# Performance work log

Measured on AMD Instinct MI355X. Metric: run time of the kernel, lower is better.

Reference implementation:

```python
import jax, jax.numpy as jnp
import numpy as np

KS = 3   # kernel_size = sqrt(window_size=9)
PAD = 1  # KS // 2


def _unfold(t):
    # F.unfold(t, kernel_size=3, padding=1) then view(B,C,K,HW).permute(0,3,2,1)
    # -> (B, HW, K, C), K enumerated row-major over the 3x3 window.
    B, C, H, W = t.shape
    tp = jnp.pad(t, ((0, 0), (0, 0), (PAD, PAD), (PAD, PAD)))
    patches = jnp.stack(
        [tp[:, :, i:i + H, j:j + W] for i in range(KS) for j in range(KS)],
        axis=2,
    )  # (B, C, K, H, W)
    return patches.reshape(B, C, KS * KS, H * W).transpose(0, 3, 2, 1)


def setup_inputs() -> dict:
    key = jax.random.key(0)
    ks = jax.random.split(key, 8)
    B, C, H, W = 8, 256, 64, 64
    Cr = C // 8  # reduction=8
    return {
        "x": jax.random.normal(ks[0], (B, C, H, W), dtype=jnp.float32),
        "Wq": jax.random.normal(ks[1], (Cr, C), dtype=jnp.float32) * 0.02,
        "bq": jax.random.normal(ks[2], (Cr,), dtype=jnp.float32) * 0.02,
        "Wk": jax.random.normal(ks[3], (Cr, C), dtype=jnp.float32) * 0.02,
        "bk": jax.random.normal(ks[4], (Cr,), dtype=jnp.float32) * 0.02,
        "Wv": jax.random.normal(ks[5], (C, C), dtype=jnp.float32) * 0.02,
        "bv": jax.random.normal(ks[6], (C,), dtype=jnp.float32) * 0.02,
        "gamma": jax.random.normal(ks[7], (1,), dtype=jnp.float32) * 0.1,
    }


def reference(x, Wq, bq, Wk, bk, Wv, bv, gamma):
    B, C, H, W = x.shape
    # 1x1 convs == per-pixel linear projections
    q = jnp.einsum('bchw,oc->bohw', x, Wq) + bq[None, :, None, None]
    k = jnp.einsum('bchw,oc->bohw', x, Wk) + bk[None, :, None, None]
    v = jnp.einsum('bchw,oc->bohw', x, Wv) + bv[None, :, None, None]
    ku = _unfold(k)  # (B, HW, K, Cr)
    vu = _unfold(v)  # (B, HW, K, C)
    qf = q.reshape(B, -1, H * W).transpose(0, 2, 1)  # (B, HW, Cr)
    energy = jnp.einsum('bqc,bqkc->bqk', qf, ku)     # (B, HW, K)
    attn = jax.nn.softmax(energy, axis=-1)
    out = jnp.einsum('bqk,bqkc->bqc', attn, vu)      # (B, HW, C)
    out = out.transpose(0, 2, 1).reshape(B, C, H, W)
    return gamma * out + x
```

## Files before the change

### kernel.cpp

```cpp
#include <hip/hip_runtime.h>

#define HW   4096
#define HIMG 64
#define WIMG 64
#define CC   256
#define CR   32
#define B_   8

typedef __attribute__((ext_vector_type(8))) short bf16x8;
typedef __attribute__((ext_vector_type(4))) float f32x4;

__device__ inline unsigned short f2bf(float f) {
    union { float f; unsigned u; } v; v.f = f;
    return (unsigned short)((v.u + 0x8000u) >> 16);
}
__device__ inline float bf2f(unsigned short h) {
    union { unsigned u; float f; } v; v.u = ((unsigned)h) << 16; return v.f;
}
__device__ inline unsigned pack2(float a, float b) {
    return (unsigned)f2bf(a) | ((unsigned)f2bf(b) << 16);
}

__global__ __launch_bounds__(256) void wconv(
    const float* __restrict__ Wq, const float* __restrict__ bq,
    const float* __restrict__ Wk, const float* __restrict__ bk,
    const float* __restrict__ Wv, const float* __restrict__ bv,
    unsigned short* __restrict__ Wb, float* __restrict__ bb)
{
    const int o = blockIdx.x;
    const float* src; const float* bsrc; int orel;
    if (o < 32)      { src = Wq; bsrc = bq; orel = o;      }
    else if (o < 64) { src = Wk; bsrc = bk; orel = o - 32; }
    else             { src = Wv; bsrc = bv; orel = o - 64; }
    Wb[o * CC + threadIdx.x] = f2bf(src[orel * CC + threadIdx.x]);
    if (threadIdx.x == 0) bb[o] = bsrc[orel];
}

__global__ __launch_bounds__(256) void proj_gemm(
    const unsigned short* __restrict__ Wb, const float* __restrict__ bb,
    const float* __restrict__ x,
    float* __restrict__ q, float* __restrict__ k,
    unsigned short* __restrict__ vv)
{
    __shared__ unsigned short As[320 * 72];
    __shared__ float          xt32[64 * 65];
    __shared__ unsigned short Bs[64 * 64];

    const int b   = blockIdx.y;
    const int hw0 = blockIdx.x * 64;
    const int t    = threadIdx.x;
    const int lane = t & 63, wv = t >> 6;
    const int m16  = lane & 15, quad = lane >> 4;

    f32x4 acc[5][4];
    #pragma unroll
    for (int i = 0; i < 5; ++i)
        #pragma unroll
        for (int n = 0; n < 4; ++n)
            acc[i][n] = (f32x4){0.f, 0.f, 0.f, 0.f};

    for (int kc = 0; kc < 4; ++kc) {
        const int k0 = kc * 64;
        if (kc) __syncthreads();

        #pragma unroll
        for (int i = 0; i < 10; ++i) {
            int idx = t + 256 * i;
            int row = idx >> 3, s8 = idx & 7;
            *(uint4*)&As[row * 72 + s8 * 8] =
                *(const uint4*)&Wb[row * CC + k0 + s8 * 8];
        }
        #pragma unroll
        for (int i = 0; i < 4; ++i) {
            int idx = t + 256 * i;
            int c = idx >> 4, p4 = (idx & 15) * 4;
            float4 vx = *(const float4*)&x[((size_t)b * CC + k0 + c) * HW + hw0 + p4];
            *(float4*)&xt32[c * 65 + p4] = vx;
        }
        __syncthreads();

        {
            const int px = lane;
            const int c0 = wv * 16;
            float f[16];
            #pragma unroll
            for (int j = 0; j < 16; ++j)
                f[j] = xt32[(c0 + j) * 65 + px];
            uint4 w0, w1;
            w0.x = pack2(f[0],  f[1]);  w0.y = pack2(f[2],  f[3]);
            w0.z = pack2(f[4],  f[5]);  w0.w = pack2(f[6],  f[7]);
            w1.x = pack2(f[8],  f[9]);  w1.y = pack2(f[10], f[11]);
            w1.z = pack2(f[12], f[13]); w1.w = pack2(f[14], f[15]);
            const int lg0 = c0 >> 3, sw = px & 7;
            *(uint4*)&Bs[px * 64 + ((lg0     ^ sw) * 8)] = w0;
            *(uint4*)&Bs[px * 64 + (((lg0+1) ^ sw) * 8)] = w1;
        }
        __syncthreads();

        #pragma unroll
        for (int ks = 0; ks < 2; ++ks) {
            bf16x8 af[5], bf[4];
            #pragma unroll
            for (int i = 0; i < 5; ++i)
                af[i] = *(const bf16x8*)&As[((wv * 5 + i) * 16 + m16) * 72
                                            + ks * 32 + quad * 8];
            #pragma unroll
            for (int n = 0; n < 4; ++n) {
                int px = n * 16 + m16;
                int lg = ks * 4 + quad;
                bf[n] = *(const bf16x8*)&Bs[px * 64 + ((lg ^ (px & 7)) * 8)];
            }
            #pragma unroll
            for (int i = 0; i < 5; ++i)
                #pragma unroll
                for (int n = 0; n < 4; ++n)
                    acc[i][n] = __builtin_amdgcn_mfma_f32_16x16x32_bf16(
                        af[i], bf[n], acc[i][n], 0, 0, 0);
        }
    }

    #pragma unroll
    for (int i = 0; i < 5; ++i) {
        const int ob = (wv * 5 + i) * 16;
        #pragma unroll
        for (int r = 0; r < 4; ++r) {
            const int orow = quad * 4 + r;
            const float bias = bb[ob + orow];
            if (ob < 64) {
                float* dst = (ob < 32) ? q : k;
                int orel = (ob < 32) ? ob : ob - 32;
                size_t rowbase = ((size_t)b * CR + orel + orow) * HW;
                #pragma unroll
                for (int n = 0; n < 4; ++n)
                    dst[rowbase + hw0 + n * 16 + m16] = acc[i][n][r] + bias;
            } else {
                size_t rowbase = ((size_t)b * CC + (ob - 64) + orow) * HW;
                #pragma unroll
                for (int n = 0; n < 4; ++n)
                    vv[rowbase + hw0 + n * 16 + m16] = f2bf(acc[i][n][r] + bias);
            }
        }
    }
}

__global__ __launch_bounds__(256) void attn_w(
    const float* __restrict__ q_, const float* __restrict__ k_,
    float* __restrict__ aw)
{
    __shared__ float qs[64][33];
    __shared__ float ks[3][64][33];
    __shared__ float es[64][9];
    const int h = blockIdx.x, b = blockIdx.y, t = threadIdx.x;

    #pragma unroll
    for (int i = 0; i < 2; ++i) {
        int idx = t + 256 * i, cr = idx >> 4, p4 = (idx & 15) * 4;
        float4 vq = *(const float4*)&q_[((size_t)b * CR + cr) * HW + h * WIMG + p4];
        qs[p4 + 0][cr] = vq.x; qs[p4 + 1][cr] = vq.y;
        qs[p4 + 2][cr] = vq.z; qs[p4 + 3][cr] = vq.w;
    }
    #pragma unroll
    for (int r = 0; r < 3; ++r) {
        int hh = h + r - 1;
        bool ok = (hh >= 0) && (hh < HIMG);
        #pragma unroll
        for (int i = 0; i < 2; ++i) {
            int idx = t + 256 * i, cr = idx >> 4, p4 = (idx & 15) * 4;
            float4 vk = make_float4(0.f, 0.f, 0.f, 0.f);
            if (ok)
                vk = *(const float4*)&k_[((size_t)b * CR + cr) * HW + hh * WIMG + p4];
            ks[r][p4 + 0][cr] = vk.x; ks[r][p4 + 1][cr] = vk.y;
            ks[r][p4 + 2][cr] = vk.z; ks[r][p4 + 3][cr] = vk.w;
        }
    }
    __syncthreads();

    for (int id = t; id < 576; id += 256) {
        int px = id / 9, kk = id - px * 9;
        int di = kk / 3, dj = kk - di * 3;
        int hh = h + di - 1, ww = px + dj - 1;
        float e = 0.f;
        if (hh >= 0 && hh < HIMG && ww >= 0 && ww < WIMG) {
            float s = 0.f;
            #pragma unroll
            for (int c = 0; c < CR; ++c) s = fmaf(qs[px][c], ks[di][ww][c], s);
            e = s;
        }
        es[px][kk] = e;
    }
    __syncthreads();

    if (t < 64) {
        float m = es[t][0];
        #pragma unroll
        for (int kk = 1; kk < 9; ++kk) m = fmaxf(m, es[t][kk]);
        float ex[9]; float ssum = 0.f;
        #pragma unroll
        for (int kk = 0; kk < 9; ++kk) { ex[kk] = __expf(es[t][kk] - m); ssum += ex[kk]; }
        float inv = 1.f / ssum;
        float* dst = &aw[((size_t)b * HW + h * WIMG + t) * 12];
        #pragma unroll
        for (int kk = 0; kk < 9; ++kk) dst[kk] = ex[kk] * inv;
    }
}

__global__ __launch_bounds__(256) void apply(
    const float* __restrict__ x, const unsigned short* __restrict__ vv,
    const float* __restrict__ aw, const float* __restrict__ gamma,
    float* __restrict__ out)
{
    __shared__ float vs[3][32][73];
    __shared__ float aws[64][13];
    const int h = blockIdx.x, cb = blockIdx.y, b = blockIdx.z, t = threadIdx.x;

    for (int p = t; p < 768; p += 256) {
        int px = p / 12, kk = p - px * 12;
        aws[px][kk] = aw[((size_t)b * HW + h * WIMG) * 12 + p];
    }
    #pragma unroll
    for (int i = 0; i < 6; ++i) {
        int idx = t + 256 * i;
        int p4 = (idx & 15) * 4, c = (idx >> 4) & 31, r = idx >> 9;
        int hh = h + r - 1;
        float4 val = make_float4(0.f, 0.f, 0.f, 0.f);
        if (hh >= 0 && hh < HIMG) {
            ushort4 u = *(const ushort4*)&vv[((size_t)b * CC + cb * 32 + c) * HW
                                             + hh * WIMG + p4];
            val = make_float4(bf2f(u.x), bf2f(u.y), bf2f(u.z), bf2f(u.w));
        }
        float* dstp = &vs[r][c][4 + p4];
        dstp[0] = val.x; dstp[1] = val.y; dstp[2] = val.z; dstp[3] = val.w;
    }
    if (t < 96) {
        int r = t >> 5, c = t & 31;
        float* row = &vs[r][c][0];
        row[0] = 0.f; row[1] = 0.f; row[2] = 0.f; row[3] = 0.f;
        row[68] = 0.f; row[69] = 0.f; row[70] = 0.f; row[71] = 0.f;
    }
    __syncthreads();

    const int px0 = (t & 15) * 4;
    const int cl  = t >> 4;
    float w[4][9];
    #pragma unroll
    for (int i = 0; i < 4; ++i)
        #pragma unroll
        for (int kk = 0; kk < 9; ++kk) w[i][kk] = aws[px0 + i][kk];
    const float g = gamma[0];

    #pragma unroll
    for (int ci = 0; ci < 2; ++ci) {
        int c = cl + 16 * ci;
        float a0 = 0.f, a1 = 0.f, a2 = 0.f, a3 = 0.f;
        #pragma unroll
        for (int r = 0; r < 3; ++r) {
            const float* row = &vs[r][c][0];
            float lft = row[3 + px0];
            float c0  = row[4 + px0];
            float c1  = row[5 + px0];
            float c2  = row[6 + px0];
            float c3  = row[7 + px0];
            float rgt = row[8 + px0];
            int r3 = r * 3;
            a0 = fmaf(w[0][r3], lft, fmaf(w[0][r3+1], c0, fmaf(w[0][r3+2], c1, a0)));
            a1 = fmaf(w[1][r3], c0,  fmaf(w[1][r3+1], c1, fmaf(w[1][r3+2], c2, a1)));
            a2 = fmaf(w[2][r3], c1,  fmaf(w[2][r3+1], c2, fmaf(w[2][r3+2], c3, a2)));
            a3 = fmaf(w[3][r3], c2,  fmaf(w[3][r3+1], c3, fmaf(w[3][r3+2], rgt, a3)));
        }
        size_t base = ((size_t)b * CC + cb * 32 + c) * HW + h * WIMG + px0;
        float4 xa = *(const float4*)&x[base];
        float4 o;
        o.x = fmaf(g, a0, xa.x); o.y = fmaf(g, a1, xa.y);
        o.z = fmaf(g, a2, xa.z); o.w = fmaf(g, a3, xa.w);
        *(float4*)&out[base] = o;
    }
}

extern "C" void kernel_launch(void* const* d_in, const int* in_sizes, int n_in,
                              void* d_out, int out_size, void* d_ws, size_t ws_size,
                              hipStream_t stream)
{
    const float* x     = (const float*)d_in[0];
    const float* Wq    = (const float*)d_in[1];
    const float* bq    = (const float*)d_in[2];
    const float* Wk    = (const float*)d_in[3];
    const float* bk    = (const float*)d_in[4];
    const float* Wv    = (const float*)d_in[5];
    const float* bv    = (const float*)d_in[6];
    const float* gamma = (const float*)d_in[7];
    float* out = (float*)d_out;

    float* q  = (float*)d_ws;
    float* k  = q + (size_t)B_ * CR * HW;
    unsigned short* vv = (unsigned short*)(k + (size_t)B_ * CR * HW);
    float* aw = (float*)(vv + (size_t)B_ * CC * HW);
    unsigned short* Wb = (unsigned short*)(aw + (size_t)B_ * HW * 12);
    float* bb = (float*)(Wb + 320 * CC);

    wconv<<<dim3(320), 256, 0, stream>>>(Wq, bq, Wk, bk, Wv, bv, Wb, bb);
    proj_gemm<<<dim3(HW / 64, B_), 256, 0, stream>>>(Wb, bb, x, q, k, vv);
    attn_w<<<dim3(HIMG, B_), 256, 0, stream>>>(q, k, aw);
    apply<<<dim3(HIMG, CC / 32, B_), 256, 0, stream>>>(x, vv, aw, gamma, out);
}
```

Baseline: 131.7 us.

## Prefetch x tiles into registers and swizzle block-to-row mapping across kernels

In the projection GEMM, the next 64-channel slab of x is loaded into registers while the MFMA loop runs on the current one, so global latency overlaps with compute. The apply kernel issues its residual x loads at the start, before the shared-memory staging. All three main kernels remap blockIdx.x with a bit-swizzle so consecutively scheduled blocks touch spread-out rows, changing which neighbouring rows share cache and how blocks spread across XCDs. The cost is higher register pressure from the held float4 values, which may lower occupancy.

```diff
diff --git a/kernel.cpp b/kernel.cpp
--- a/kernel.cpp
+++ b/kernel.cpp
@@ -20,6 +20,7 @@
 __device__ inline unsigned pack2(float a, float b) {
     return (unsigned)f2bf(a) | ((unsigned)f2bf(b) << 16);
 }
+__device__ inline int hswz(int hx) { return ((hx & 7) << 3) | (hx >> 3); }
 
 __global__ __launch_bounds__(256) void wconv(
     const float* __restrict__ Wq, const float* __restrict__ bq,
@@ -47,7 +48,7 @@
     __shared__ unsigned short Bs[64 * 64];
 
     const int b   = blockIdx.y;
-    const int hw0 = blockIdx.x * 64;
+    const int hw0 = hswz(blockIdx.x) * 64;
     const int t    = threadIdx.x;
     const int lane = t & 63, wv = t >> 6;
     const int m16  = lane & 15, quad = lane >> 4;
@@ -59,9 +60,22 @@
         for (int n = 0; n < 4; ++n)
             acc[i][n] = (f32x4){0.f, 0.f, 0.f, 0.f};
 
+    const int xc  = t >> 4;
+    const int xp4 = (t & 15) * 4;
+    const float* xbase = &x[((size_t)b * CC + xc) * HW + hw0 + xp4];
+
+    float4 xp[4];
+    #pragma unroll
+    for (int i = 0; i < 4; ++i)
+        xp[i] = *(const float4*)&xbase[(size_t)(16 * i) * HW];
+
     for (int kc = 0; kc < 4; ++kc) {
         const int k0 = kc * 64;
         if (kc) __syncthreads();
+
+        #pragma unroll
+        for (int i = 0; i < 4; ++i)
+            *(float4*)&xt32[(xc + 16 * i) * 65 + xp4] = xp[i];
 
         #pragma unroll
         for (int i = 0; i < 10; ++i) {
@@ -69,13 +83,6 @@
             int row = idx >> 3, s8 = idx & 7;
             *(uint4*)&As[row * 72 + s8 * 8] =
                 *(const uint4*)&Wb[row * CC + k0 + s8 * 8];
-        }
-        #pragma unroll
-        for (int i = 0; i < 4; ++i) {
-            int idx = t + 256 * i;
-            int c = idx >> 4, p4 = (idx & 15) * 4;
-            float4 vx = *(const float4*)&x[((size_t)b * CC + k0 + c) * HW + hw0 + p4];
-            *(float4*)&xt32[c * 65 + p4] = vx;
         }
         __syncthreads();
 
@@ -96,6 +103,12 @@
             *(uint4*)&Bs[px * 64 + (((lg0+1) ^ sw) * 8)] = w1;
         }
         __syncthreads();
+
+        if (kc < 3) {
+            #pragma unroll
+            for (int i = 0; i < 4; ++i)
+                xp[i] = *(const float4*)&xbase[(size_t)(k0 + 64 + 16 * i) * HW];
+        }
 
         #pragma unroll
         for (int ks = 0; ks < 2; ++ks) {
@@ -150,7 +163,7 @@
     __shared__ float qs[64][33];
     __shared__ float ks[3][64][33];
     __shared__ float es[64][9];
-    const int h = blockIdx.x, b = blockIdx.y, t = threadIdx.x;
+    const int h = hswz(blockIdx.x), b = blockIdx.y, t = threadIdx.x;
 
     #pragma unroll
     for (int i = 0; i < 2; ++i) {
@@ -211,7 +224,17 @@
 {
     __shared__ float vs[3][32][73];
     __shared__ float aws[64][13];
-    const int h = blockIdx.x, cb = blockIdx.y, b = blockIdx.z, t = threadIdx.x;
+    const int h = hswz(blockIdx.x), cb = blockIdx.y, b = blockIdx.z, t = threadIdx.x;
+
+    const int px0 = (t & 15) * 4;
+    const int cl  = t >> 4;
+    float4 xa[2]; size_t basec[2];
+    #pragma unroll
+    for (int ci = 0; ci < 2; ++ci) {
+        int c = cl + 16 * ci;
+        basec[ci] = ((size_t)b * CC + cb * 32 + c) * HW + h * WIMG + px0;
+        xa[ci] = *(const float4*)&x[basec[ci]];
+    }
 
     for (int p = t; p < 768; p += 256) {
         int px = p / 12, kk = p - px * 12;
@@ -239,8 +262,6 @@
     }
     __syncthreads();
 
-    const int px0 = (t & 15) * 4;
-    const int cl  = t >> 4;
     float w[4][9];
     #pragma unroll
     for (int i = 0; i < 4; ++i)
@@ -267,12 +288,10 @@
             a2 = fmaf(w[2][r3], c1,  fmaf(w[2][r3+1], c2, fmaf(w[2][r3+2], c3, a2)));
             a3 = fmaf(w[3][r3], c2,  fmaf(w[3][r3+1], c3, fmaf(w[3][r3+2], rgt, a3)));
         }
-        size_t base = ((size_t)b * CC + cb * 32 + c) * HW + h * WIMG + px0;
-        float4 xa = *(const float4*)&x[base];
         float4 o;
-        o.x = fmaf(g, a0, xa.x); o.y = fmaf(g, a1, xa.y);
-        o.z = fmaf(g, a2, xa.z); o.w = fmaf(g, a3, xa.w);
-        *(float4*)&out[base] = o;
+        o.x = fmaf(g, a0, xa[ci].x); o.y = fmaf(g, a1, xa[ci].y);
+        o.z = fmaf(g, a2, xa[ci].z); o.w = fmaf(g, a3, xa[ci].w);
+        *(float4*)&out[basec[ci]] = o;
     }
 }
 
```

Result: slower. 141.7 us (+7.6%).

## Fuse attention-weight softmax and value aggregation into a single kernel

Applied to the files above, without the earlier changes.

Merges the attn_w and apply kernels into one attn_apply kernel. Each 512-thread block computes the softmax weights for one image row into shared memory, then loops over four 64-channel chunks of V to produce the output. This removes the attention-weight round trip through global memory and one kernel launch. In exchange the grid shrinks from 4096 to 512 blocks, the value loads are serialized inside each block, and shared memory is reused through a union.

```diff
diff --git a/kernel.cpp b/kernel.cpp
--- a/kernel.cpp
+++ b/kernel.cpp
@@ -143,39 +143,43 @@
     }
 }
 
-__global__ __launch_bounds__(256) void attn_w(
+__global__ __launch_bounds__(512) void attn_apply(
     const float* __restrict__ q_, const float* __restrict__ k_,
-    float* __restrict__ aw)
-{
-    __shared__ float qs[64][33];
-    __shared__ float ks[3][64][33];
-    __shared__ float es[64][9];
+    const unsigned short* __restrict__ vv,
+    const float* __restrict__ x, const float* __restrict__ gamma,
+    float* __restrict__ out)
+{
+    struct PA {
+        float qs[64][33];
+        float ks[3][64][33];
+        float es[64][9];
+    };
+    struct PV {
+        float vs[3][64][73];
+    };
+    __shared__ union USM { PA a; PV v; } sm;
+    __shared__ float aws[64][13];
+
     const int h = blockIdx.x, b = blockIdx.y, t = threadIdx.x;
 
-    #pragma unroll
-    for (int i = 0; i < 2; ++i) {
-        int idx = t + 256 * i, cr = idx >> 4, p4 = (idx & 15) * 4;
+    {
+        const int cr = t >> 4, p4 = (t & 15) * 4;
         float4 vq = *(const float4*)&q_[((size_t)b * CR + cr) * HW + h * WIMG + p4];
-        qs[p4 + 0][cr] = vq.x; qs[p4 + 1][cr] = vq.y;
-        qs[p4 + 2][cr] = vq.z; qs[p4 + 3][cr] = vq.w;
-    }
-    #pragma unroll
-    for (int r = 0; r < 3; ++r) {
-        int hh = h + r - 1;
-        bool ok = (hh >= 0) && (hh < HIMG);
-        #pragma unroll
-        for (int i = 0; i < 2; ++i) {
-            int idx = t + 256 * i, cr = idx >> 4, p4 = (idx & 15) * 4;
+        sm.a.qs[p4 + 0][cr] = vq.x; sm.a.qs[p4 + 1][cr] = vq.y;
+        sm.a.qs[p4 + 2][cr] = vq.z; sm.a.qs[p4 + 3][cr] = vq.w;
+        #pragma unroll
+        for (int r = 0; r < 3; ++r) {
+            int hh = h + r - 1;
             float4 vk = make_float4(0.f, 0.f, 0.f, 0.f);
-            if (ok)
+            if (hh >= 0 && hh < HIMG)
                 vk = *(const float4*)&k_[((size_t)b * CR + cr) * HW + hh * WIMG + p4];
-            ks[r][p4 + 0][cr] = vk.x; ks[r][p4 + 1][cr] = vk.y;
-            ks[r][p4 + 2][cr] = vk.z; ks[r][p4 + 3][cr] = vk.w;
+            sm.a.ks[r][p4 + 0][cr] = vk.x; sm.a.ks[r][p4 + 1][cr] = vk.y;
+            sm.a.ks[r][p4 + 2][cr] = vk.z; sm.a.ks[r][p4 + 3][cr] = vk.w;
         }
     }
     __syncthreads();
 
-    for (int id = t; id < 576; id += 256) {
+    for (int id = t; id < 576; id += 512) {
         int px = id / 9, kk = id - px * 9;
         int di = kk / 3, dj = kk - di * 3;
         int hh = h + di - 1, ww = px + dj - 1;
@@ -183,96 +187,87 @@
         if (hh >= 0 && hh < HIMG && ww >= 0 && ww < WIMG) {
             float s = 0.f;
             #pragma unroll
-            for (int c = 0; c < CR; ++c) s = fmaf(qs[px][c], ks[di][ww][c], s);
+            for (int c = 0; c < CR; ++c)
+                s = fmaf(sm.a.qs[px][c], sm.a.ks[di][ww][c], s);
             e = s;
         }
-        es[px][kk] = e;
+        sm.a.es[px][kk] = e;
     }
     __syncthreads();
 
     if (t < 64) {
-        float m = es[t][0];
-        #pragma unroll
-        for (int kk = 1; kk < 9; ++kk) m = fmaxf(m, es[t][kk]);
+        float m = sm.a.es[t][0];
+        #pragma unroll
+        for (int kk = 1; kk < 9; ++kk) m = fmaxf(m, sm.a.es[t][kk]);
         float ex[9]; float ssum = 0.f;
         #pragma unroll
-        for (int kk = 0; kk < 9; ++kk) { ex[kk] = __expf(es[t][kk] - m); ssum += ex[kk]; }
+        for (int kk = 0; kk < 9; ++kk) { ex[kk] = __expf(sm.a.es[t][kk] - m); ssum += ex[kk]; }
         float inv = 1.f / ssum;
-        float* dst = &aw[((size_t)b * HW + h * WIMG + t) * 12];
-        #pragma unroll
-        for (int kk = 0; kk < 9; ++kk) dst[kk] = ex[kk] * inv;
-    }
-}
-
-__global__ __launch_bounds__(256) void apply(
-    const float* __restrict__ x, const unsigned short* __restrict__ vv,
-    const float* __restrict__ aw, const float* __restrict__ gamma,
-    float* __restrict__ out)
-{
-    __shared__ float vs[3][32][73];
-    __shared__ float aws[64][13];
-    const int h = blockIdx.x, cb = blockIdx.y, b = blockIdx.z, t = threadIdx.x;
-
-    for (int p = t; p < 768; p += 256) {
-        int px = p / 12, kk = p - px * 12;
-        aws[px][kk] = aw[((size_t)b * HW + h * WIMG) * 12 + p];
-    }
-    #pragma unroll
-    for (int i = 0; i < 6; ++i) {
-        int idx = t + 256 * i;
-        int p4 = (idx & 15) * 4, c = (idx >> 4) & 31, r = idx >> 9;
-        int hh = h + r - 1;
-        float4 val = make_float4(0.f, 0.f, 0.f, 0.f);
-        if (hh >= 0 && hh < HIMG) {
-            ushort4 u = *(const ushort4*)&vv[((size_t)b * CC + cb * 32 + c) * HW
-                                             + hh * WIMG + p4];
-            val = make_float4(bf2f(u.x), bf2f(u.y), bf2f(u.z), bf2f(u.w));
-        }
-        float* dstp = &vs[r][c][4 + p4];
-        dstp[0] = val.x; dstp[1] = val.y; dstp[2] = val.z; dstp[3] = val.w;
-    }
-    if (t < 96) {
-        int r = t >> 5, c = t & 31;
-        float* row = &vs[r][c][0];
+        #pragma unroll
+        for (int kk = 0; kk < 9; ++kk) aws[t][kk] = ex[kk] * inv;
+    }
+    __syncthreads();
+
+    if (t < 192) {
+        int r = t / 64, c = t - r * 64;
+        float* row = &sm.v.vs[r][c][0];
         row[0] = 0.f; row[1] = 0.f; row[2] = 0.f; row[3] = 0.f;
         row[68] = 0.f; row[69] = 0.f; row[70] = 0.f; row[71] = 0.f;
     }
-    __syncthreads();
 
     const int px0 = (t & 15) * 4;
     const int cl  = t >> 4;
+    const float g = gamma[0];
     float w[4][9];
     #pragma unroll
     for (int i = 0; i < 4; ++i)
         #pragma unroll
         for (int kk = 0; kk < 9; ++kk) w[i][kk] = aws[px0 + i][kk];
-    const float g = gamma[0];
-
-    #pragma unroll
-    for (int ci = 0; ci < 2; ++ci) {
-        int c = cl + 16 * ci;
-        float a0 = 0.f, a1 = 0.f, a2 = 0.f, a3 = 0.f;
-        #pragma unroll
-        for (int r = 0; r < 3; ++r) {
-            const float* row = &vs[r][c][0];
-            float lft = row[3 + px0];
-            float c0  = row[4 + px0];
-            float c1  = row[5 + px0];
-            float c2  = row[6 + px0];
-            float c3  = row[7 + px0];
-            float rgt = row[8 + px0];
-            int r3 = r * 3;
-            a0 = fmaf(w[0][r3], lft, fmaf(w[0][r3+1], c0, fmaf(w[0][r3+2], c1, a0)));
-            a1 = fmaf(w[1][r3], c0,  fmaf(w[1][r3+1], c1, fmaf(w[1][r3+2], c2, a1)));
-            a2 = fmaf(w[2][r3], c1,  fmaf(w[2][r3+1], c2, fmaf(w[2][r3+2], c3, a2)));
-            a3 = fmaf(w[3][r3], c2,  fmaf(w[3][r3+1], c3, fmaf(w[3][r3+2], rgt, a3)));
-        }
-        size_t base = ((size_t)b * CC + cb * 32 + c) * HW + h * WIMG + px0;
-        float4 xa = *(const float4*)&x[base];
-        float4 o;
-        o.x = fmaf(g, a0, xa.x); o.y = fmaf(g, a1, xa.y);
-        o.z = fmaf(g, a2, xa.z); o.w = fmaf(g, a3, xa.w);
-        *(float4*)&out[base] = o;
+
+    for (int cb = 0; cb < 4; ++cb) {
+        if (cb) __syncthreads();
+        #pragma unroll
+        for (int i = 0; i < 6; ++i) {
+            int idx = t + 512 * i;
+            int p4 = (idx & 15) * 4, c = (idx >> 4) & 63, r = idx >> 10;
+            int hh = h + r - 1;
+            float4 val = make_float4(0.f, 0.f, 0.f, 0.f);
+            if (hh >= 0 && hh < HIMG) {
+                ushort4 u = *(const ushort4*)&vv[((size_t)b * CC + cb * 64 + c) * HW
+                                                 + hh * WIMG + p4];
+                val = make_float4(bf2f(u.x), bf2f(u.y), bf2f(u.z), bf2f(u.w));
+            }
+            float* dstp = &sm.v.vs[r][c][4 + p4];
+            dstp[0] = val.x; dstp[1] = val.y; dstp[2] = val.z; dstp[3] = val.w;
+        }
+        __syncthreads();
+
+        #pragma unroll
+        for (int ci = 0; ci < 2; ++ci) {
+            int c = cl + 32 * ci;
+            float a0 = 0.f, a1 = 0.f, a2 = 0.f, a3 = 0.f;
+            #pragma unroll
+            for (int r = 0; r < 3; ++r) {
+                const float* row = &sm.v.vs[r][c][0];
+                float lft = row[3 + px0];
+                float c0  = row[4 + px0];
+                float c1  = row[5 + px0];
+                float c2  = row[6 + px0];
+                float c3  = row[7 + px0];
+                float rgt = row[8 + px0];
+                int r3 = r * 3;
+                a0 = fmaf(w[0][r3], lft, fmaf(w[0][r3+1], c0, fmaf(w[0][r3+2], c1, a0)));
+                a1 = fmaf(w[1][r3], c0,  fmaf(w[1][r3+1], c1, fmaf(w[1][r3+2], c2, a1)));
+                a2 = fmaf(w[2][r3], c1,  fmaf(w[2][r3+1], c2, fmaf(w[2][r3+2], c3, a2)));
+                a3 = fmaf(w[3][r3], c2,  fmaf(w[3][r3+1], c3, fmaf(w[3][r3+2], rgt, a3)));
+            }
+            size_t base = ((size_t)b * CC + cb * 64 + c) * HW + h * WIMG + px0;
+            float4 xa = *(const float4*)&x[base];
+            float4 o;
+            o.x = fmaf(g, a0, xa.x); o.y = fmaf(g, a1, xa.y);
+            o.z = fmaf(g, a2, xa.z); o.w = fmaf(g, a3, xa.w);
+            *(float4*)&out[base] = o;
+        }
     }
 }
 
@@ -293,12 +288,10 @@
     float* q  = (float*)d_ws;
     float* k  = q + (size_t)B_ * CR * HW;
     unsigned short* vv = (unsigned short*)(k + (size_t)B_ * CR * HW);
-    float* aw = (float*)(vv + (size_t)B_ * CC * HW);
-    unsigned short* Wb = (unsigned short*)(aw + (size_t)B_ * HW * 12);
+    unsigned short* Wb = vv + (size_t)B_ * CC * HW;
     float* bb = (float*)(Wb + 320 * CC);
 
     wconv<<<dim3(320), 256, 0, stream>>>(Wq, bq, Wk, bk, Wv, bv, Wb, bb);
     proj_gemm<<<dim3(HW / 64, B_), 256, 0, stream>>>(Wb, bb, x, q, k, vv);
-    attn_w<<<dim3(HIMG, B_), 256, 0, stream>>>(q, k, aw);
-    apply<<<dim3(HIMG, CC / 32, B_), 256, 0, stream>>>(x, vv, aw, gamma, out);
-}
+    attn_apply<<<dim3(HIMG, B_), 512, 0, stream>>>(q, k, vv, x, gamma, out);
+}
```

Measured after the change: 128.8 us. 2.2% less time.
